# Performance work log

Measured on AMD Instinct MI355X. Metric: run time of the kernel, lower is better.

Reference implementation:

```python
import jax, jax.numpy as jnp
import numpy as np

H = 16
QK_NOPE = 128
QK_ROPE = 64
QK_HEAD = 192
V_HEAD = 128
KV_LORA = 512
Q_LORA = 1536
HIDDEN = 2048
ROPE_THETA = 500000.0
EPS = 1e-6


def _rms_norm(x, w, eps=EPS):
    var = jnp.mean(x * x, axis=-1, keepdims=True)
    return w * (x * jax.lax.rsqrt(var + eps))


def _rotate_half(x):
    d = x.shape[-1] // 2
    return jnp.concatenate([-x[..., d:], x[..., :d]], axis=-1)


def _rope_cos_sin(T, dim, theta, dtype):
    inv_freq = 1.0 / (theta ** (jnp.arange(0, dim, 2, dtype=jnp.float32) / dim))
    t = jnp.arange(T, dtype=jnp.float32)
    freqs = jnp.outer(t, inv_freq)               # [T, dim//2]
    emb = jnp.concatenate([freqs, freqs], axis=-1)  # [T, dim]
    return jnp.cos(emb).astype(dtype), jnp.sin(emb).astype(dtype)


def _apply_rope_interleave(q, k, cos, sin):
    # deinterleave: [x0,x1,x2,...] -> [x0,x2,... , x1,x3,...]
    def deint(x):
        return jnp.concatenate([x[..., 0::2], x[..., 1::2]], axis=-1)
    q, k = deint(q), deint(k)
    cos = cos[None, None]  # [1,1,T,d]
    sin = sin[None, None]
    q_e = q * cos + _rotate_half(q) * sin
    k_e = k * cos + _rotate_half(k) * sin
    return q_e, k_e


def setup_inputs() -> dict:
    key = jax.random.key(0)
    ks = jax.random.split(key, 8)
    s = 0.02
    B, T = 2, 2048
    return {
        "x": jax.random.normal(ks[0], (B, T, HIDDEN), jnp.float32),
        "q_a_w": jax.random.normal(ks[1], (HIDDEN, Q_LORA), jnp.float32) * s,
        "q_a_ln_w": jnp.ones((Q_LORA,), jnp.float32),
        "q_b_w": jax.random.normal(ks[2], (Q_LORA, H * QK_HEAD), jnp.float32) * s,
        "kv_a_w": jax.random.normal(ks[3], (HIDDEN, KV_LORA + QK_ROPE), jnp.float32) * s,
        "kv_a_ln_w": jnp.ones((KV_LORA,), jnp.float32),
        "kv_b_w": jax.random.normal(ks[4], (KV_LORA, H * (QK_NOPE + V_HEAD)), jnp.float32) * s,
        "o_w": jax.random.normal(ks[5], (H * V_HEAD, HIDDEN), jnp.float32) * s,
    }


def reference(x, q_a_w, q_a_ln_w, q_b_w, kv_a_w, kv_a_ln_w, kv_b_w, o_w):
    B, T, _ = x.shape
    scale = QK_HEAD ** -0.5

    # Q path: hidden -> q_lora -> RMSNorm -> H*qk_head
    q = _rms_norm(x @ q_a_w, q_a_ln_w) @ q_b_w
    q = q.reshape(B, T, H, QK_HEAD).transpose(0, 2, 1, 3)  # [B,H,T,qk_head]
    q_nope, q_rope = q[..., :QK_NOPE], q[..., QK_NOPE:]

    # KV path: hidden -> kv_lora + rope_dim
    ckv = x @ kv_a_w
    kv_c, k_rope = ckv[..., :KV_LORA], ckv[..., KV_LORA:]
    kv = _rms_norm(kv_c, kv_a_ln_w) @ kv_b_w
    kv = kv.reshape(B, T, H, QK_NOPE + V_HEAD).transpose(0, 2, 1, 3)
    k_nope, v = kv[..., :QK_NOPE], kv[..., QK_NOPE:]

    k_rope = k_rope.reshape(B, 1, T, QK_ROPE)
    cos, sin = _rope_cos_sin(T, QK_ROPE, ROPE_THETA, x.dtype)
    q_rope, k_rope = _apply_rope_interleave(q_rope, k_rope, cos, sin)
    k_rope = jnp.broadcast_to(k_rope, (B, H, T, QK_ROPE))

    qf = jnp.concatenate([q_nope, q_rope], axis=-1)  # [B,H,T,192]
    kf = jnp.concatenate([k_nope, k_rope], axis=-1)

    # causal SDPA
    scores = jnp.einsum("bhqd,bhkd->bhqk", qf, kf) * scale
    causal = jnp.tril(jnp.ones((T, T), bool))
    scores = jnp.where(causal[None, None], scores, jnp.finfo(scores.dtype).min)
    attn = jax.nn.softmax(scores, axis=-1)
    out = jnp.einsum("bhqk,bhkd->bhqd", attn, v)  # [B,H,T,128]
    out = out.transpose(0, 2, 1, 3).reshape(B, T, H * V_HEAD)
    return out @ o_w
```

## Files before the change

kernel.cpp:

```cpp
#include <hip/hip_runtime.h>
#include <hip/hip_bf16.h>
#include <cstdint>


typedef __bf16 bf16;
typedef __bf16 bf16x8 __attribute__((ext_vector_type(8)));
typedef __bf16 bf16x4v __attribute__((ext_vector_type(4)));
typedef float f32x4 __attribute__((ext_vector_type(4)));

#define TSEQ 2048
#define MR 4096

typedef const uint32_t __attribute__((address_space(1))) * gas1_t;
typedef uint32_t __attribute__((address_space(3))) * las3_t;

static __device__ __forceinline__ void gload_lds16(const void* g, void* l) {
  __builtin_amdgcn_global_load_lds(
      reinterpret_cast<gas1_t>(reinterpret_cast<uintptr_t>(g)),
      reinterpret_cast<las3_t>(reinterpret_cast<uintptr_t>(l)), 16, 0, 0);
}

static __device__ __forceinline__ f32x4 mfma16(bf16x8 a, bf16x8 b, f32x4 c) {
  return __builtin_amdgcn_mfma_f32_16x16x32_bf16(a, b, c, 0, 0, 0);
}

static __device__ __forceinline__ void do_transpose(
    const float* __restrict__ W, bf16* __restrict__ Wt, int K, int N, int bi,
    int bj, float (*t)[33]) {
  int c = threadIdx.x & 31, r0 = threadIdx.x >> 5;
#pragma unroll
  for (int rr = 0; rr < 32; rr += 8)
    t[rr + r0][c] = W[(size_t)(bj * 32 + rr + r0) * N + bi * 32 + c];
  __syncthreads();
#pragma unroll
  for (int rr = 0; rr < 32; rr += 8)
    Wt[(size_t)(bi * 32 + rr + r0) * K + bj * 32 + c] = (bf16)t[c][rr + r0];
}

#define PREP_BLOCKS (8192 + 3072 + 1152 + 4608 + 2048 + 4096 + 192 + 256)

__global__ __launch_bounds__(256) void k_prep(
    const float* __restrict__ x, const float* __restrict__ q_a_w,
    const float* __restrict__ kv_a_w, const float* __restrict__ q_b_w,
    const float* __restrict__ kv_b_w, const float* __restrict__ o_w,
    bf16* __restrict__ x_bf, bf16* __restrict__ ab_wt,
    bf16* __restrict__ qb_wt, bf16* __restrict__ kvb_wt,
    bf16* __restrict__ o_wt, float* __restrict__ rt) {
  __shared__ float t[32][33];
  int nb = blockIdx.x;
  const int tid = threadIdx.x;
  if (nb < 8192) {
    int i = nb * 256 + tid;
    float4 f = reinterpret_cast<const float4*>(x)[i];
    bf16x4v o = {(bf16)f.x, (bf16)f.y, (bf16)f.z, (bf16)f.w};
    reinterpret_cast<bf16x4v*>(x_bf)[i] = o;
    return;
  }
  nb -= 8192;
  if (nb < 3072) { do_transpose(q_a_w, ab_wt, 2048, 1536, nb % 48, nb / 48, t); return; }
  nb -= 3072;
  if (nb < 1152) {
    do_transpose(kv_a_w, ab_wt + (size_t)1536 * 2048, 2048, 576, nb % 18, nb / 18, t);
    return;
  }
  nb -= 1152;
  if (nb < 4608) { do_transpose(q_b_w, qb_wt, 1536, 3072, nb % 96, nb / 96, t); return; }
  nb -= 4608;
  if (nb < 2048) { do_transpose(kv_b_w, kvb_wt, 512, 4096, nb % 128, nb / 128, t); return; }
  nb -= 2048;
  if (nb < 4096) { do_transpose(o_w, o_wt, 2048, 2048, nb % 64, nb / 64, t); return; }
  nb -= 4096;
  if (nb < 192) {
    uint4 z = make_uint4(0, 0, 0, 0);
    reinterpret_cast<uint4*>(ab_wt + (size_t)2112 * 2048)[nb * 256 + tid] = z;
    return;
  }
  nb -= 192;
  {
    int idx = nb * 256 + tid;
    int tt = idx >> 5, j = idx & 31;
    float freq = exp2f(-(float)j * (1.0f / 32.0f) * log2f(500000.0f));
    float ang = (float)tt * freq;
    rt[tt * 64 + 2 * j] = cosf(ang);
    rt[tt * 64 + 2 * j + 1] = sinf(ang);
  }
}

__global__ __launch_bounds__(64) void k_norms(
    const bf16* __restrict__ qac, const float* __restrict__ qw,
    const float* __restrict__ kvw, const float* __restrict__ rt,
    bf16* __restrict__ q_a_n, bf16* __restrict__ kv_c_n,
    bf16* __restrict__ kr) {
  int row = blockIdx.x, lane = threadIdx.x;
  const bf16* ip = qac + (size_t)row * 2304;
  bf16x8 v[3];
  float ss = 0.f;
#pragma unroll
  for (int c = 0; c < 3; ++c) {
    v[c] = *reinterpret_cast<const bf16x8*>(ip + c * 512 + lane * 8);
#pragma unroll
    for (int e = 0; e < 8; ++e) { float f = (float)v[c][e]; ss += f * f; }
  }
#pragma unroll
  for (int m = 1; m <= 32; m <<= 1) ss += __shfl_xor(ss, m);
  float rs = rsqrtf(ss / 1536.0f + 1e-6f);
  bf16* op = q_a_n + (size_t)row * 1536;
#pragma unroll
  for (int c = 0; c < 3; ++c) {
    bf16x8 o;
#pragma unroll
    for (int e = 0; e < 8; ++e)
      o[e] = (bf16)((float)v[c][e] * rs * qw[c * 512 + lane * 8 + e]);
    *reinterpret_cast<bf16x8*>(op + c * 512 + lane * 8) = o;
  }
  bf16x8 kvv = *reinterpret_cast<const bf16x8*>(ip + 1536 + lane * 8);
  float s2 = 0.f;
#pragma unroll
  for (int e = 0; e < 8; ++e) { float f = (float)kvv[e]; s2 += f * f; }
#pragma unroll
  for (int m = 1; m <= 32; m <<= 1) s2 += __shfl_xor(s2, m);
  float rs2 = rsqrtf(s2 / 512.0f + 1e-6f);
  bf16x8 o2;
#pragma unroll
  for (int e = 0; e < 8; ++e)
    o2[e] = (bf16)((float)kvv[e] * rs2 * kvw[lane * 8 + e]);
  *reinterpret_cast<bf16x8*>(kv_c_n + (size_t)row * 512 + lane * 8) = o2;
  if (lane < 32) {
    int t = row & (TSEQ - 1);
    float x0 = (float)ip[2048 + 2 * lane], x1 = (float)ip[2048 + 2 * lane + 1];
    float c = rt[t * 64 + 2 * lane], s = rt[t * 64 + 2 * lane + 1];
    kr[(size_t)row * 64 + lane] = (bf16)(x0 * c - x1 * s);
    kr[(size_t)row * 64 + 32 + lane] = (bf16)(x1 * c + x0 * s);
  }
}

__global__ __launch_bounds__(256) void k_rope_q(const bf16* __restrict__ q,
                                                const float* __restrict__ rt,
                                                bf16* __restrict__ qr) {
  int idx = blockIdx.x * 256 + threadIdx.x;
  int j = idx & 31, h = (idx >> 5) & 15, row = idx >> 9;
  int t = row & (TSEQ - 1);
  const bf16* src = q + (size_t)row * 3072 + h * 192 + 128;
  float x0 = (float)src[2 * j], x1 = (float)src[2 * j + 1];
  float c = rt[t * 64 + 2 * j], s = rt[t * 64 + 2 * j + 1];
  bf16* dst = qr + ((size_t)row * 16 + h) * 64;
  dst[j] = (bf16)(x0 * c - x1 * s);
  dst[32 + j] = (bf16)(x1 * c + x0 * s);
}

#define GPH(BUF, MH, KH, DO_READB, STAGE_STMT, WAIT_STMT)                     \
  {                                                                           \
    if (DO_READB) {                                                           \
      _Pragma("unroll") for (int ni = 0; ni < 4; ++ni) {                      \
        int row = wn * 64 + ni * 16 + lr;                                     \
        breg[KH][ni] = *reinterpret_cast<const bf16x8*>(                      \
            &Bs[BUF][row * 64 + ((((KH)*4 + lg) ^ (row & 7)) * 8)]);          \
      }                                                                       \
    }                                                                         \
    bf16x8 af[4];                                                             \
    _Pragma("unroll") for (int mi = 0; mi < 4; ++mi) {                        \
      int row = wm * 128 + (MH)*64 + mi * 16 + lr;                            \
      af[mi] = *reinterpret_cast<const bf16x8*>(                              \
          &As[BUF][row * 64 + ((((KH)*4 + lg) ^ (row & 7)) * 8)]);            \
    }                                                                         \
    STAGE_STMT;                                                               \
    __builtin_amdgcn_s_barrier();                                             \
    __builtin_amdgcn_s_setprio(1);                                            \
    _Pragma("unroll") for (int mi = 0; mi < 4; ++mi)                          \
        _Pragma("unroll") for (int ni = 0; ni < 4; ++ni)                      \
            acc[(MH)*4 + mi][ni] =                                            \
        mfma16(af[mi], breg[KH][ni], acc[(MH)*4 + mi][ni]);                   \
    __builtin_amdgcn_s_setprio(0);                                            \
    WAIT_STMT;                                                                \
    __builtin_amdgcn_s_barrier();                                             \
  }

template <bool OUT_F32>
static __device__ __forceinline__ void gemm8_body(
    const bf16* __restrict__ A, const bf16* __restrict__ Bt,
    void* __restrict__ C, int N, int K, int bi, int bj, bf16 (*As)[16384],
    bf16 (*Bs)[16384]) {
  const int tid = threadIdx.x, lane = tid & 63, w = tid >> 6;
  const int lg = lane >> 4, lr = lane & 15;
  const int wm = w >> 2, wn = w & 3;
  const int m0 = bj * 256, n0 = bi * 256;
  const int T = K >> 7;

  f32x4 acc[8][4] = {};
  bf16x8 breg[2][4];

  auto stageA = [&](int tau, int h) {
    char* dst = (char*)&As[tau & 1][0] + h * 16384;
#pragma unroll
    for (int j = 0; j < 2; ++j) {
      int c = j * 512 + tid;
      int row = c >> 3, slot = c & 7;
      gload_lds16(A + (size_t)(m0 + h * 128 + row) * K + tau * 64 +
                      ((slot ^ (row & 7)) * 8),
                  dst + (size_t)(j * 512 + w * 64) * 16);
    }
  };
  auto stageB = [&](int tau, int h) {
    char* dst = (char*)&Bs[tau & 1][0] + h * 16384;
#pragma unroll
    for (int j = 0; j < 2; ++j) {
      int c = j * 512 + tid;
      int row = c >> 3, slot = c & 7;
      gload_lds16(Bt + (size_t)(n0 + h * 128 + row) * K + tau * 64 +
                      ((slot ^ (row & 7)) * 8),
                  dst + (size_t)(j * 512 + w * 64) * 16);
    }
  };

  stageB(0, 0); stageB(0, 1); stageA(0, 0); stageA(0, 1);
  stageB(1, 0); stageB(1, 1); stageA(1, 0);
  asm volatile("s_waitcnt vmcnt(6)" ::: "memory");
  __builtin_amdgcn_s_barrier();

  for (int t = 0; t < T - 1; ++t) {
    const int s2 = 2 * t + 2, s3 = 2 * t + 3, a1 = 2 * t + 1;
    GPH(0, 0, 0, true,  stageA(a1, 1), ((void)0));
    GPH(0, 0, 1, true,  stageB(s2, 0), ((void)0));
    GPH(0, 1, 0, false, stageB(s2, 1), ((void)0));
    GPH(0, 1, 1, false, stageA(s2, 0),
        asm volatile("s_waitcnt vmcnt(6)" ::: "memory"));
    GPH(1, 0, 0, true,  stageA(s2, 1), ((void)0));
    GPH(1, 0, 1, true,  stageB(s3, 0), ((void)0));
    GPH(1, 1, 0, false, stageB(s3, 1), ((void)0));
    GPH(1, 1, 1, false, stageA(s3, 0),
        asm volatile("s_waitcnt vmcnt(6)" ::: "memory"));
  }
  {
    const int a1 = 2 * T - 1;
    GPH(0, 0, 0, true,  stageA(a1, 1), ((void)0));
    GPH(0, 0, 1, true,  ((void)0),     ((void)0));
    GPH(0, 1, 0, false, ((void)0),     ((void)0));
    GPH(0, 1, 1, false, ((void)0),
        asm volatile("s_waitcnt vmcnt(0)" ::: "memory"));
    GPH(1, 0, 0, true,  ((void)0), ((void)0));
    GPH(1, 0, 1, true,  ((void)0), ((void)0));
    GPH(1, 1, 0, false, ((void)0), ((void)0));
    GPH(1, 1, 1, false, ((void)0), ((void)0));
  }

#pragma unroll
  for (int mi = 0; mi < 8; ++mi)
#pragma unroll
    for (int ni = 0; ni < 4; ++ni) {
      int col = n0 + wn * 64 + ni * 16 + lr;
#pragma unroll
      for (int r = 0; r < 4; ++r) {
        int rowg = m0 + wm * 128 + mi * 16 + lg * 4 + r;
        if (OUT_F32)
          reinterpret_cast<float*>(C)[(size_t)rowg * N + col] = acc[mi][ni][r];
        else
          reinterpret_cast<bf16*>(C)[(size_t)rowg * N + col] =
              (bf16)acc[mi][ni][r];
      }
    }
}

template <bool OUT_F32>
__global__ __launch_bounds__(512, 2) void k_gemm8(const bf16* __restrict__ A,
                                                  const bf16* __restrict__ Bt,
                                                  void* __restrict__ C, int N,
                                                  int K) {
  __shared__ bf16 As[2][16384];
  __shared__ bf16 Bs[2][16384];
  const int nwg = gridDim.x * gridDim.y;
  const int orig = blockIdx.y * gridDim.x + blockIdx.x;
  const int wgid = (orig & 7) * (nwg >> 3) + (orig >> 3);
  gemm8_body<OUT_F32>(A, Bt, C, N, K, wgid % gridDim.x, wgid / gridDim.x, As,
                      Bs);
}

__global__ __launch_bounds__(512, 2) void k_gemm8_dual(
    const bf16* __restrict__ A1, const bf16* __restrict__ B1,
    bf16* __restrict__ C1, const bf16* __restrict__ A2,
    const bf16* __restrict__ B2, bf16* __restrict__ C2) {
  __shared__ bf16 As[2][16384];
  __shared__ bf16 Bs[2][16384];
  int id = blockIdx.x;
  if (id < 192) {
    int wg = (id & 7) * 24 + (id >> 3);
    gemm8_body<false>(A1, B1, C1, 3072, 1536, wg % 12, wg / 12, As, Bs);
  } else {
    int s = id - 192;
    int wg = (s & 7) * 32 + (s >> 3);
    gemm8_body<false>(A2, B2, C2, 4096, 512, wg % 16, wg / 16, As, Bs);
  }
}

__global__ __launch_bounds__(512, 2) void k_attn(const bf16* __restrict__ q,
                                                 const bf16* __restrict__ qr,
                                                 const bf16* __restrict__ kv,
                                                 const bf16* __restrict__ kr,
                                                 bf16* __restrict__ o) {
  __shared__ bf16 Kn[2][64 * 128];
  __shared__ bf16 Kr[2][64 * 64];
  __shared__ bf16 Vs[2][64 * 128];
  __shared__ bf16 Ps[8 * 1024];
  const int tid = threadIdx.x, lane = tid & 63, w = tid >> 6;
  const int lg = lane >> 4, lr = lane & 15;
  const float qsc = 0.07216878364870323f * 1.44269504088896f;
  uint4 vreg[2];
  const int vrr = tid & 31, vvc = tid >> 5;

  for (int t = 0; t < 2; ++t) {
    const int id = t ? 511 - (int)blockIdx.x : (int)blockIdx.x;
    const int qt = 15 - (id >> 5);
    const int bh = id & 31;
    const int b = bh >> 4, h = bh & 15;
    const int q0 = qt * 128;
    const size_t rowbase = (size_t)b * TSEQ;
    const int nkt = 2 * qt + 2;
    const int qg = q0 + w * 16 + lr;

    auto issue_loads = [&](int kbase, int buf) {
#pragma unroll
      for (int kk = 0; kk < 2; ++kk)
        vreg[kk] = *reinterpret_cast<const uint4*>(
            kv + (rowbase + kbase + vrr * 2 + kk) * 4096 + h * 256 + 128 +
            vvc * 8);
#pragma unroll
      for (int i = 0; i < 2; ++i) {
        int c = i * 512 + tid;
        int row = c >> 4, j = c & 15;
        gload_lds16(
            kv + (rowbase + kbase + row) * 4096 + h * 256 +
                ((j ^ (row & 15)) * 8),
            (char*)&Kn[buf][0] + (size_t)(i * 512 + w * 64) * 16);
      }
      {
        int row = tid >> 3, j = tid & 7;
        gload_lds16(kr + (rowbase + kbase + row) * 64 + ((j ^ (row & 7)) * 8),
                    (char*)&Kr[buf][0] + (size_t)(w * 64) * 16);
      }
    };

    auto write_vs = [&](int buf) {
      const int kb0 = vrr * 2;
      const int cC = kb0 >> 5, g = (kb0 >> 3) & 3, j0 = kb0 & 7;
      const uint32_t* r0 = reinterpret_cast<const uint32_t*>(&vreg[0]);
      const uint32_t* r1 = reinterpret_cast<const uint32_t*>(&vreg[1]);
#pragma unroll
      for (int e = 0; e < 8; ++e) {
        uint32_t h0 = (r0[e >> 1] >> ((e & 1) * 16)) & 0xffffu;
        uint32_t h1 = (r1[e >> 1] >> ((e & 1) * 16)) & 0xffffu;
        int vd = vvc * 8 + e;
        int slot = (vd & 15) ^ g;
        *reinterpret_cast<uint32_t*>(
            &Vs[buf][((cC * 8 + (vd >> 4)) * 4 + g) * 128 + slot * 8 + j0]) =
            h0 | (h1 << 16);
      }
    };

    bf16x8 qf[6];
    {
      const bf16* qp = q + (rowbase + qg) * 3072 + h * 192;
#pragma unroll
      for (int dc = 0; dc < 4; ++dc) {
        bf16x8 v = *reinterpret_cast<const bf16x8*>(qp + dc * 32 + lg * 8);
#pragma unroll
        for (int e = 0; e < 8; ++e) v[e] = (bf16)((float)v[e] * qsc);
        qf[dc] = v;
      }
      const bf16* qrp = qr + ((rowbase + qg) * 16 + h) * 64;
#pragma unroll
      for (int dc = 0; dc < 2; ++dc) {
        bf16x8 v = *reinterpret_cast<const bf16x8*>(qrp + dc * 32 + lg * 8);
#pragma unroll
        for (int e = 0; e < 8; ++e) v[e] = (bf16)((float)v[e] * qsc);
        qf[4 + dc] = v;
      }
    }

    f32x4 oacc[8] = {};
    float m_run = -1e30f, l_run = 0.f;

    issue_loads(0, 0);
    write_vs(0);
    __syncthreads();

    for (int kt = 0; kt < nkt; ++kt) {
      const int kbase = kt * 64;
      const int buf = kt & 1;
      const bool more = (kt + 1 < nkt);
      if (more) issue_loads(kbase + 64, buf ^ 1);

      if (kbase <= q0 + w * 16 + 15) {
        f32x4 sacc[4];
#pragma unroll
        for (int kb = 0; kb < 4; ++kb) {
          const int row = kb * 16 + lr;
          bf16x8 kf[6];
#pragma unroll
          for (int dc = 0; dc < 4; ++dc)
            kf[dc] = *reinterpret_cast<const bf16x8*>(
                &Kn[buf][row * 128 + (((dc * 4 + lg) ^ (row & 15)) * 8)]);
#pragma unroll
          for (int dc = 0; dc < 2; ++dc)
            kf[4 + dc] = *reinterpret_cast<const bf16x8*>(
                &Kr[buf][row * 64 + (((dc * 4 + lg) ^ (row & 7)) * 8)]);
          __builtin_amdgcn_s_setprio(1);
          f32x4 sa = {0.f, 0.f, 0.f, 0.f};
#pragma unroll
          for (int dc = 0; dc < 6; ++dc) sa = mfma16(kf[dc], qf[dc], sa);
          sacc[kb] = sa;
          __builtin_amdgcn_s_setprio(0);
        }
        float sv[4][4];
        if (kbase + 63 <= q0 + w * 16) {
#pragma unroll
          for (int kb = 0; kb < 4; ++kb)
#pragma unroll
            for (int r = 0; r < 4; ++r) sv[kb][r] = sacc[kb][r];
        } else {
#pragma unroll
          for (int kb = 0; kb < 4; ++kb)
#pragma unroll
            for (int r = 0; r < 4; ++r) {
              int kgl = kbase + kb * 16 + lg * 4 + r;
              sv[kb][r] = (kgl <= qg) ? sacc[kb][r] : -1e30f;
            }
        }
        float pmax = -1e30f;
#pragma unroll
        for (int kb = 0; kb < 4; ++kb)
#pragma unroll
          for (int r = 0; r < 4; ++r) pmax = fmaxf(pmax, sv[kb][r]);
        pmax = fmaxf(pmax, __shfl_xor(pmax, 16));
        pmax = fmaxf(pmax, __shfl_xor(pmax, 32));
        if (!__all(pmax - m_run <= 8.0f)) {
          float mnew = fmaxf(m_run, pmax);
          float alpha = exp2f(m_run - mnew);
          l_run *= alpha;
#pragma unroll
          for (int vb = 0; vb < 8; ++vb) {
            oacc[vb][0] *= alpha; oacc[vb][1] *= alpha;
            oacc[vb][2] *= alpha; oacc[vb][3] *= alpha;
          }
          m_run = mnew;
        }
        float ls = 0.f;
#pragma unroll
        for (int kb = 0; kb < 4; ++kb) {
          bf16x4v pw;
#pragma unroll
          for (int r = 0; r < 4; ++r) {
            float p = exp2f(sv[kb][r] - m_run);
            ls += p;
            pw[r] = (bf16)p;
          }
          *reinterpret_cast<bf16x4v*>(
              &Ps[w * 1024 + lr * 64 +
                  (((kb * 2 + (lg >> 1)) ^ (lr & 7)) * 8) + (lg & 1) * 4]) = pw;
        }
        ls += __shfl_xor(ls, 16);
        ls += __shfl_xor(ls, 32);
        l_run += ls;
#pragma unroll
        for (int c = 0; c < 2; ++c) {
          bf16x8 pb = *reinterpret_cast<const bf16x8*>(
              &Ps[w * 1024 + lr * 64 + (((c * 4 + lg) ^ (lr & 7)) * 8)]);
          __builtin_amdgcn_s_setprio(1);
#pragma unroll
          for (int vb = 0; vb < 8; ++vb) {
            bf16x8 av = *reinterpret_cast<const bf16x8*>(
                &Vs[buf][((c * 8 + vb) * 4 + lg) * 128 + (lr ^ lg) * 8]);
            oacc[vb] = mfma16(av, pb, oacc[vb]);
          }
          __builtin_amdgcn_s_setprio(0);
        }
      }
      if (more) write_vs(buf ^ 1);
      __syncthreads();
    }

    bf16* Os = &Kn[0][0] + w * 2048;
    {
      float inv = 1.0f / l_run;
#pragma unroll
      for (int vb = 0; vb < 8; ++vb) {
        bf16x4v ov;
#pragma unroll
        for (int r = 0; r < 4; ++r) ov[r] = (bf16)(oacc[vb][r] * inv);
        int slot16 = vb * 2 + (lg >> 1);
        *reinterpret_cast<bf16x4v*>(
            &Os[lr * 128 + ((slot16 ^ (lr & 7)) * 8) + (lg & 1) * 4]) = ov;
      }
    }
    asm volatile("s_waitcnt lgkmcnt(0)");
    __builtin_amdgcn_sched_barrier(0);
#pragma unroll
    for (int i = 0; i < 4; ++i) {
      const int r = i * 4 + lg;
      bf16x8 ov = *reinterpret_cast<const bf16x8*>(
          &Os[r * 128 + ((lr ^ (r & 7)) * 8)]);
      *reinterpret_cast<bf16x8*>(
          o + (rowbase + q0 + w * 16 + r) * 2048 + h * 128 + lr * 8) = ov;
    }
    __syncthreads();
  }
}

extern "C" void kernel_launch(void* const* d_in, const int* in_sizes, int n_in,
                              void* d_out, int out_size, void* d_ws,
                              size_t ws_size, hipStream_t stream) {
  (void)in_sizes; (void)n_in; (void)out_size; (void)ws_size;
  const float* x       = (const float*)d_in[0];
  const float* q_a_w   = (const float*)d_in[1];
  const float* q_a_ln  = (const float*)d_in[2];
  const float* q_b_w   = (const float*)d_in[3];
  const float* kv_a_w  = (const float*)d_in[4];
  const float* kv_a_ln = (const float*)d_in[5];
  const float* kv_b_w  = (const float*)d_in[6];
  const float* o_w     = (const float*)d_in[7];

  char* ws = (char*)d_ws;
  size_t off = 0;
  auto alloc = [&](size_t bytes) {
    void* p = ws + off;
    off += (bytes + 255) & ~(size_t)255;
    return p;
  };
  bf16* x_bf   = (bf16*)alloc((size_t)MR * 2048 * 2);
  bf16* ab_wt  = (bf16*)alloc((size_t)2304 * 2048 * 2);
  bf16* qb_wt  = (bf16*)alloc((size_t)3072 * 1536 * 2);
  bf16* kvb_wt = (bf16*)alloc((size_t)4096 * 512 * 2);
  bf16* o_wt   = (bf16*)alloc((size_t)2048 * 2048 * 2);
  float* rt    = (float*)alloc((size_t)2048 * 64 * 4);
  bf16* qac    = (bf16*)alloc((size_t)MR * 2304 * 2);
  bf16* q_a_n  = (bf16*)alloc((size_t)MR * 1536 * 2);
  bf16* kv_c_n = (bf16*)alloc((size_t)MR * 512 * 2);
  bf16* kr     = (bf16*)alloc((size_t)MR * 64 * 2);
  bf16* qbuf   = (bf16*)alloc((size_t)MR * 3072 * 2);
  bf16* qr     = (bf16*)alloc((size_t)MR * 16 * 64 * 2);
  bf16* kvbuf  = (bf16*)alloc((size_t)MR * 4096 * 2);
  bf16* attn_o = (bf16*)alloc((size_t)MR * 2048 * 2);

  k_prep<<<PREP_BLOCKS, 256, 0, stream>>>(x, q_a_w, kv_a_w, q_b_w, kv_b_w,
                                          o_w, x_bf, ab_wt, qb_wt, kvb_wt,
                                          o_wt, rt);
  k_gemm8<false><<<dim3(9, 16), 512, 0, stream>>>(x_bf, ab_wt, qac, 2304, 2048);
  k_norms<<<MR, 64, 0, stream>>>(qac, q_a_ln, kv_a_ln, rt, q_a_n, kv_c_n, kr);
  k_gemm8_dual<<<dim3(448), 512, 0, stream>>>(q_a_n, qb_wt, qbuf, kv_c_n,
                                              kvb_wt, kvbuf);
  k_rope_q<<<8192, 256, 0, stream>>>(qbuf, rt, qr);
  k_attn<<<dim3(256), 512, 0, stream>>>(qbuf, qr, kvbuf, kr, attn_o);
  k_gemm8<true><<<dim3(8, 16), 512, 0, stream>>>(attn_o, o_wt, d_out, 2048, 2048);
}
```

Baseline: 278.4 us.

## Launch one attention tile per block and cut LDS to raise occupancy

The attention kernel no longer loops over two paired q-tiles per block. It launches 512 blocks, each owning one tile, with a new mapping that interleaves heavy and light causal tiles. Kr and Vs drop from double to single buffering, and Kr is now staged through registers instead of direct global-to-LDS loads. Launch bounds rise to 4 blocks per CU so more blocks can be resident. The smaller LDS footprint buys occupancy, at the cost of an extra barrier per iteration and less explicit load balancing inside a block.

```diff
diff --git a/kernel.cpp b/kernel.cpp
--- a/kernel.cpp
+++ b/kernel.cpp
@@ -291,216 +291,213 @@
   }
 }
 
-__global__ __launch_bounds__(512, 2) void k_attn(const bf16* __restrict__ q,
+__global__ __launch_bounds__(512, 4) void k_attn(const bf16* __restrict__ q,
                                                  const bf16* __restrict__ qr,
                                                  const bf16* __restrict__ kv,
                                                  const bf16* __restrict__ kr,
                                                  bf16* __restrict__ o) {
   __shared__ bf16 Kn[2][64 * 128];
-  __shared__ bf16 Kr[2][64 * 64];
-  __shared__ bf16 Vs[2][64 * 128];
+  __shared__ bf16 Kr[64 * 64];
+  __shared__ bf16 Vs[64 * 128];
   __shared__ bf16 Ps[8 * 1024];
   const int tid = threadIdx.x, lane = tid & 63, w = tid >> 6;
   const int lg = lane >> 4, lr = lane & 15;
   const float qsc = 0.07216878364870323f * 1.44269504088896f;
-  uint4 vreg[2];
+  uint4 vreg[2], krreg;
   const int vrr = tid & 31, vvc = tid >> 5;
-
-  for (int t = 0; t < 2; ++t) {
-    const int id = t ? 511 - (int)blockIdx.x : (int)blockIdx.x;
-    const int qt = 15 - (id >> 5);
-    const int bh = id & 31;
-    const int b = bh >> 4, h = bh & 15;
-    const int q0 = qt * 128;
-    const size_t rowbase = (size_t)b * TSEQ;
-    const int nkt = 2 * qt + 2;
-    const int qg = q0 + w * 16 + lr;
-
-    auto issue_loads = [&](int kbase, int buf) {
-#pragma unroll
-      for (int kk = 0; kk < 2; ++kk)
-        vreg[kk] = *reinterpret_cast<const uint4*>(
-            kv + (rowbase + kbase + vrr * 2 + kk) * 4096 + h * 256 + 128 +
-            vvc * 8);
-#pragma unroll
-      for (int i = 0; i < 2; ++i) {
-        int c = i * 512 + tid;
-        int row = c >> 4, j = c & 15;
-        gload_lds16(
-            kv + (rowbase + kbase + row) * 4096 + h * 256 +
-                ((j ^ (row & 15)) * 8),
-            (char*)&Kn[buf][0] + (size_t)(i * 512 + w * 64) * 16);
+  const int krrow = tid >> 3, krj = tid & 7;
+
+  const int id = (int)blockIdx.x;
+  const int qt = (id < 256) ? (15 - 2 * (id >> 5)) : (2 * ((id - 256) >> 5));
+  const int bh = id & 31;
+  const int b = bh >> 4, h = bh & 15;
+  const int q0 = qt * 128;
+  const size_t rowbase = (size_t)b * TSEQ;
+  const int nkt = 2 * qt + 2;
+  const int qg = q0 + w * 16 + lr;
+
+  auto issue_loads = [&](int kbase, int buf) {
+#pragma unroll
+    for (int kk = 0; kk < 2; ++kk)
+      vreg[kk] = *reinterpret_cast<const uint4*>(
+          kv + (rowbase + kbase + vrr * 2 + kk) * 4096 + h * 256 + 128 +
+          vvc * 8);
+    krreg = *reinterpret_cast<const uint4*>(
+        kr + (rowbase + kbase + krrow) * 64 + ((krj ^ (krrow & 7)) * 8));
+#pragma unroll
+    for (int i = 0; i < 2; ++i) {
+      int c = i * 512 + tid;
+      int row = c >> 4, j = c & 15;
+      gload_lds16(
+          kv + (rowbase + kbase + row) * 4096 + h * 256 +
+              ((j ^ (row & 15)) * 8),
+          (char*)&Kn[buf][0] + (size_t)(i * 512 + w * 64) * 16);
+    }
+  };
+
+  auto write_stage = [&]() {
+    *reinterpret_cast<uint4*>(&Kr[tid * 8]) = krreg;
+    const int kb0 = vrr * 2;
+    const int cC = kb0 >> 5, g = (kb0 >> 3) & 3, j0 = kb0 & 7;
+    const uint32_t* r0 = reinterpret_cast<const uint32_t*>(&vreg[0]);
+    const uint32_t* r1 = reinterpret_cast<const uint32_t*>(&vreg[1]);
+#pragma unroll
+    for (int e = 0; e < 8; ++e) {
+      uint32_t h0 = (r0[e >> 1] >> ((e & 1) * 16)) & 0xffffu;
+      uint32_t h1 = (r1[e >> 1] >> ((e & 1) * 16)) & 0xffffu;
+      int vd = vvc * 8 + e;
+      int slot = (vd & 15) ^ g;
+      *reinterpret_cast<uint32_t*>(
+          &Vs[((cC * 8 + (vd >> 4)) * 4 + g) * 128 + slot * 8 + j0]) =
+          h0 | (h1 << 16);
+    }
+  };
+
+  bf16x8 qf[6];
+  {
+    const bf16* qp = q + (rowbase + qg) * 3072 + h * 192;
+#pragma unroll
+    for (int dc = 0; dc < 4; ++dc) {
+      bf16x8 v = *reinterpret_cast<const bf16x8*>(qp + dc * 32 + lg * 8);
+#pragma unroll
+      for (int e = 0; e < 8; ++e) v[e] = (bf16)((float)v[e] * qsc);
+      qf[dc] = v;
+    }
+    const bf16* qrp = qr + ((rowbase + qg) * 16 + h) * 64;
+#pragma unroll
+    for (int dc = 0; dc < 2; ++dc) {
+      bf16x8 v = *reinterpret_cast<const bf16x8*>(qrp + dc * 32 + lg * 8);
+#pragma unroll
+      for (int e = 0; e < 8; ++e) v[e] = (bf16)((float)v[e] * qsc);
+      qf[4 + dc] = v;
+    }
+  }
+
+  f32x4 oacc[8] = {};
+  float m_run = -1e30f, l_run = 0.f;
+
+  issue_loads(0, 0);
+  write_stage();
+  __syncthreads();
+
+  for (int kt = 0; kt < nkt; ++kt) {
+    const int kbase = kt * 64;
+    const int buf = kt & 1;
+    const bool more = (kt + 1 < nkt);
+    if (more) issue_loads(kbase + 64, buf ^ 1);
+
+    if (kbase <= q0 + w * 16 + 15) {
+      f32x4 sacc[4];
+#pragma unroll
+      for (int kb = 0; kb < 4; ++kb) {
+        const int row = kb * 16 + lr;
+        bf16x8 kf[6];
+#pragma unroll
+        for (int dc = 0; dc < 4; ++dc)
+          kf[dc] = *reinterpret_cast<const bf16x8*>(
+              &Kn[buf][row * 128 + (((dc * 4 + lg) ^ (row & 15)) * 8)]);
+#pragma unroll
+        for (int dc = 0; dc < 2; ++dc)
+          kf[4 + dc] = *reinterpret_cast<const bf16x8*>(
+              &Kr[row * 64 + (((dc * 4 + lg) ^ (row & 7)) * 8)]);
+        __builtin_amdgcn_s_setprio(1);
+        f32x4 sa = {0.f, 0.f, 0.f, 0.f};
+#pragma unroll
+        for (int dc = 0; dc < 6; ++dc) sa = mfma16(kf[dc], qf[dc], sa);
+        sacc[kb] = sa;
+        __builtin_amdgcn_s_setprio(0);
       }
-      {
-        int row = tid >> 3, j = tid & 7;
-        gload_lds16(kr + (rowbase + kbase + row) * 64 + ((j ^ (row & 7)) * 8),
-                    (char*)&Kr[buf][0] + (size_t)(w * 64) * 16);
+      float sv[4][4];
+      if (kbase + 63 <= q0 + w * 16) {
+#pragma unroll
+        for (int kb = 0; kb < 4; ++kb)
+#pragma unroll
+          for (int r = 0; r < 4; ++r) sv[kb][r] = sacc[kb][r];
+      } else {
+#pragma unroll
+        for (int kb = 0; kb < 4; ++kb)
+#pragma unroll
+          for (int r = 0; r < 4; ++r) {
+            int kgl = kbase + kb * 16 + lg * 4 + r;
+            sv[kb][r] = (kgl <= qg) ? sacc[kb][r] : -1e30f;
+          }
       }
-    };
-
-    auto write_vs = [&](int buf) {
-      const int kb0 = vrr * 2;
-      const int cC = kb0 >> 5, g = (kb0 >> 3) & 3, j0 = kb0 & 7;
-      const uint32_t* r0 = reinterpret_cast<const uint32_t*>(&vreg[0]);
-      const uint32_t* r1 = reinterpret_cast<const uint32_t*>(&vreg[1]);
-#pragma unroll
-      for (int e = 0; e < 8; ++e) {
-        uint32_t h0 = (r0[e >> 1] >> ((e & 1) * 16)) & 0xffffu;
-        uint32_t h1 = (r1[e >> 1] >> ((e & 1) * 16)) & 0xffffu;
-        int vd = vvc * 8 + e;
-        int slot = (vd & 15) ^ g;
-        *reinterpret_cast<uint32_t*>(
-            &Vs[buf][((cC * 8 + (vd >> 4)) * 4 + g) * 128 + slot * 8 + j0]) =
-            h0 | (h1 << 16);
+      float pmax = -1e30f;
+#pragma unroll
+      for (int kb = 0; kb < 4; ++kb)
+#pragma unroll
+        for (int r = 0; r < 4; ++r) pmax = fmaxf(pmax, sv[kb][r]);
+      pmax = fmaxf(pmax, __shfl_xor(pmax, 16));
+      pmax = fmaxf(pmax, __shfl_xor(pmax, 32));
+      if (!__all(pmax - m_run <= 8.0f)) {
+        float mnew = fmaxf(m_run, pmax);
+        float alpha = exp2f(m_run - mnew);
+        l_run *= alpha;
+#pragma unroll
+        for (int vb = 0; vb < 8; ++vb) {
+          oacc[vb][0] *= alpha; oacc[vb][1] *= alpha;
+          oacc[vb][2] *= alpha; oacc[vb][3] *= alpha;
+        }
+        m_run = mnew;
       }
-    };
-
-    bf16x8 qf[6];
-    {
-      const bf16* qp = q + (rowbase + qg) * 3072 + h * 192;
-#pragma unroll
-      for (int dc = 0; dc < 4; ++dc) {
-        bf16x8 v = *reinterpret_cast<const bf16x8*>(qp + dc * 32 + lg * 8);
-#pragma unroll
-        for (int e = 0; e < 8; ++e) v[e] = (bf16)((float)v[e] * qsc);
-        qf[dc] = v;
+      float ls = 0.f;
+#pragma unroll
+      for (int kb = 0; kb < 4; ++kb) {
+        bf16x4v pw;
+#pragma unroll
+        for (int r = 0; r < 4; ++r) {
+          float p = exp2f(sv[kb][r] - m_run);
+          ls += p;
+          pw[r] = (bf16)p;
+        }
+        *reinterpret_cast<bf16x4v*>(
+            &Ps[w * 1024 + lr * 64 +
+                (((kb * 2 + (lg >> 1)) ^ (lr & 7)) * 8) + (lg & 1) * 4]) = pw;
       }
-      const bf16* qrp = qr + ((rowbase + qg) * 16 + h) * 64;
-#pragma unroll
-      for (int dc = 0; dc < 2; ++dc) {
-        bf16x8 v = *reinterpret_cast<const bf16x8*>(qrp + dc * 32 + lg * 8);
-#pragma unroll
-        for (int e = 0; e < 8; ++e) v[e] = (bf16)((float)v[e] * qsc);
-        qf[4 + dc] = v;
+      ls += __shfl_xor(ls, 16);
+      ls += __shfl_xor(ls, 32);
+      l_run += ls;
+#pragma unroll
+      for (int c = 0; c < 2; ++c) {
+        bf16x8 pb = *reinterpret_cast<const bf16x8*>(
+            &Ps[w * 1024 + lr * 64 + (((c * 4 + lg) ^ (lr & 7)) * 8)]);
+        __builtin_amdgcn_s_setprio(1);
+#pragma unroll
+        for (int vb = 0; vb < 8; ++vb) {
+          bf16x8 av = *reinterpret_cast<const bf16x8*>(
+              &Vs[((c * 8 + vb) * 4 + lg) * 128 + (lr ^ lg) * 8]);
+          oacc[vb] = mfma16(av, pb, oacc[vb]);
+        }
+        __builtin_amdgcn_s_setprio(0);
       }
     }
-
-    f32x4 oacc[8] = {};
-    float m_run = -1e30f, l_run = 0.f;
-
-    issue_loads(0, 0);
-    write_vs(0);
     __syncthreads();
-
-    for (int kt = 0; kt < nkt; ++kt) {
-      const int kbase = kt * 64;
-      const int buf = kt & 1;
-      const bool more = (kt + 1 < nkt);
-      if (more) issue_loads(kbase + 64, buf ^ 1);
-
-      if (kbase <= q0 + w * 16 + 15) {
-        f32x4 sacc[4];
-#pragma unroll
-        for (int kb = 0; kb < 4; ++kb) {
-          const int row = kb * 16 + lr;
-          bf16x8 kf[6];
-#pragma unroll
-          for (int dc = 0; dc < 4; ++dc)
-            kf[dc] = *reinterpret_cast<const bf16x8*>(
-                &Kn[buf][row * 128 + (((dc * 4 + lg) ^ (row & 15)) * 8)]);
-#pragma unroll
-          for (int dc = 0; dc < 2; ++dc)
-            kf[4 + dc] = *reinterpret_cast<const bf16x8*>(
-                &Kr[buf][row * 64 + (((dc * 4 + lg) ^ (row & 7)) * 8)]);
-          __builtin_amdgcn_s_setprio(1);
-          f32x4 sa = {0.f, 0.f, 0.f, 0.f};
-#pragma unroll
-          for (int dc = 0; dc < 6; ++dc) sa = mfma16(kf[dc], qf[dc], sa);
-          sacc[kb] = sa;
-          __builtin_amdgcn_s_setprio(0);
-        }
-        float sv[4][4];
-        if (kbase + 63 <= q0 + w * 16) {
-#pragma unroll
-          for (int kb = 0; kb < 4; ++kb)
-#pragma unroll
-            for (int r = 0; r < 4; ++r) sv[kb][r] = sacc[kb][r];
-        } else {
-#pragma unroll
-          for (int kb = 0; kb < 4; ++kb)
-#pragma unroll
-            for (int r = 0; r < 4; ++r) {
-              int kgl = kbase + kb * 16 + lg * 4 + r;
-              sv[kb][r] = (kgl <= qg) ? sacc[kb][r] : -1e30f;
-            }
-        }
-        float pmax = -1e30f;
-#pragma unroll
-        for (int kb = 0; kb < 4; ++kb)
-#pragma unroll
-          for (int r = 0; r < 4; ++r) pmax = fmaxf(pmax, sv[kb][r]);
-        pmax = fmaxf(pmax, __shfl_xor(pmax, 16));
-        pmax = fmaxf(pmax, __shfl_xor(pmax, 32));
-        if (!__all(pmax - m_run <= 8.0f)) {
-          float mnew = fmaxf(m_run, pmax);
-          float alpha = exp2f(m_run - mnew);
-          l_run *= alpha;
-#pragma unroll
-          for (int vb = 0; vb < 8; ++vb) {
-            oacc[vb][0] *= alpha; oacc[vb][1] *= alpha;
-            oacc[vb][2] *= alpha; oacc[vb][3] *= alpha;
-          }
-          m_run = mnew;
-        }
-        float ls = 0.f;
-#pragma unroll
-        for (int kb = 0; kb < 4; ++kb) {
-          bf16x4v pw;
-#pragma unroll
-          for (int r = 0; r < 4; ++r) {
-            float p = exp2f(sv[kb][r] - m_run);
-            ls += p;
-            pw[r] = (bf16)p;
-          }
-          *reinterpret_cast<bf16x4v*>(
-              &Ps[w * 1024 + lr * 64 +
-                  (((kb * 2 + (lg >> 1)) ^ (lr & 7)) * 8) + (lg & 1) * 4]) = pw;
-        }
-        ls += __shfl_xor(ls, 16);
-        ls += __shfl_xor(ls, 32);
-        l_run += ls;
-#pragma unroll
-        for (int c = 0; c < 2; ++c) {
-          bf16x8 pb = *reinterpret_cast<const bf16x8*>(
-              &Ps[w * 1024 + lr * 64 + (((c * 4 + lg) ^ (lr & 7)) * 8)]);
-          __builtin_amdgcn_s_setprio(1);
-#pragma unroll
-          for (int vb = 0; vb < 8; ++vb) {
-            bf16x8 av = *reinterpret_cast<const bf16x8*>(
-                &Vs[buf][((c * 8 + vb) * 4 + lg) * 128 + (lr ^ lg) * 8]);
-            oacc[vb] = mfma16(av, pb, oacc[vb]);
-          }
-          __builtin_amdgcn_s_setprio(0);
-        }
-      }
-      if (more) write_vs(buf ^ 1);
-      __syncthreads();
-    }
-
-    bf16* Os = &Kn[0][0] + w * 2048;
-    {
-      float inv = 1.0f / l_run;
-#pragma unroll
-      for (int vb = 0; vb < 8; ++vb) {
-        bf16x4v ov;
-#pragma unroll
-        for (int r = 0; r < 4; ++r) ov[r] = (bf16)(oacc[vb][r] * inv);
-        int slot16 = vb * 2 + (lg >> 1);
-        *reinterpret_cast<bf16x4v*>(
-            &Os[lr * 128 + ((slot16 ^ (lr & 7)) * 8) + (lg & 1) * 4]) = ov;
-      }
-    }
-    asm volatile("s_waitcnt lgkmcnt(0)");
-    __builtin_amdgcn_sched_barrier(0);
-#pragma unroll
-    for (int i = 0; i < 4; ++i) {
-      const int r = i * 4 + lg;
-      bf16x8 ov = *reinterpret_cast<const bf16x8*>(
-          &Os[r * 128 + ((lr ^ (r & 7)) * 8)]);
-      *reinterpret_cast<bf16x8*>(
-          o + (rowbase + q0 + w * 16 + r) * 2048 + h * 128 + lr * 8) = ov;
-    }
+    if (more) write_stage();
     __syncthreads();
+  }
+
+  bf16* Os = &Kn[0][0] + w * 2048;
+  {
+    float inv = 1.0f / l_run;
+#pragma unroll
+    for (int vb = 0; vb < 8; ++vb) {
+      bf16x4v ov;
+#pragma unroll
+      for (int r = 0; r < 4; ++r) ov[r] = (bf16)(oacc[vb][r] * inv);
+      int slot16 = vb * 2 + (lg >> 1);
+      *reinterpret_cast<bf16x4v*>(
+          &Os[lr * 128 + ((slot16 ^ (lr & 7)) * 8) + (lg & 1) * 4]) = ov;
+    }
+  }
+  asm volatile("s_waitcnt lgkmcnt(0)");
+  __builtin_amdgcn_sched_barrier(0);
+#pragma unroll
+  for (int i = 0; i < 4; ++i) {
+    const int r = i * 4 + lg;
+    bf16x8 ov = *reinterpret_cast<const bf16x8*>(
+        &Os[r * 128 + ((lr ^ (r & 7)) * 8)]);
+    *reinterpret_cast<bf16x8*>(
+        o + (rowbase + q0 + w * 16 + r) * 2048 + h * 128 + lr * 8) = ov;
   }
 }
 
@@ -547,6 +544,6 @@
   k_gemm8_dual<<<dim3(448), 512, 0, stream>>>(q_a_n, qb_wt, qbuf, kv_c_n,
                                               kvb_wt, kvbuf);
   k_rope_q<<<8192, 256, 0, stream>>>(qbuf, rt, qr);
-  k_attn<<<dim3(256), 512, 0, stream>>>(qbuf, qr, kvbuf, kr, attn_o);
+  k_attn<<<dim3(512), 512, 0, stream>>>(qbuf, qr, kvbuf, kr, attn_o);
   k_gemm8<true><<<dim3(8, 16), 512, 0, stream>>>(attn_o, o_wt, d_out, 2048, 2048);
 }
```

Result: slower. 489.3 us (+75.7%).
